# Kernel optimization log

Measured on AMD Instinct MI355X. Metric: run time of the kernel, lower is better.

## Reference

```python
import jax, jax.numpy as jnp
import numpy as np

N_NODES = 50000
N_EDGES = 1600000
IN_F = 512
OUT_F = 256


def setup_inputs() -> dict:
    key = jax.random.key(0)
    k1, k2, k3, k4, k5 = jax.random.split(key, 5)
    features = jax.random.normal(k1, (N_NODES, IN_F), dtype=jnp.float32)
    # xavier_uniform init for weight [in_features, out_features]
    limit = np.sqrt(6.0 / (IN_F + OUT_F)).astype(np.float32)
    weight = jax.random.uniform(k2, (IN_F, OUT_F), dtype=jnp.float32,
                                minval=-limit, maxval=limit)
    # COO sparse adjacency (normalized edge weights in [0,1))
    edge_vals = jax.random.uniform(k3, (N_EDGES,), dtype=jnp.float32)
    edge_rows = jax.random.randint(k4, (N_EDGES,), 0, N_NODES, dtype=jnp.int32)
    edge_cols = jax.random.randint(k5, (N_EDGES,), 0, N_NODES, dtype=jnp.int32)
    return {"features": features, "weight": weight, "edge_vals": edge_vals,
            "edge_rows": edge_rows, "edge_cols": edge_cols}


def reference(features, weight, edge_vals, edge_rows, edge_cols):
    # dropout p=0.0 / eval mode -> identity
    support = features @ weight                      # [N, out_f] dense GEMM
    # torch.spmm(adj, support): out[r] += val * support[c] for each edge (r, c)
    gathered = support[edge_cols] * edge_vals[:, None]   # [E, out_f]
    output = jax.ops.segment_sum(gathered, edge_rows, num_segments=N_NODES)
    return jax.nn.relu(output)
```

## Files before the change

kernel.cpp:

```cpp
#include <hip/hip_runtime.h>

#define N_NODES 50000
#define N_EDGES 1600000
#define IN_F    512
#define OUT_F   256

#define BROWS   128
#define NBINS   ((N_NODES + BROWS - 1) / BROWS)
#define BATCH   4096
#define NBATCHES ((N_EDGES + BATCH - 1) / BATCH)
#define EPT     (BATCH / 256)

typedef __attribute__((ext_vector_type(8))) short bf16x8;
typedef __attribute__((ext_vector_type(4))) float f32x4;
typedef unsigned long long ull;

__device__ __forceinline__ short bf16rne(float f) {
    unsigned u = __builtin_bit_cast(unsigned, f);
    u += 0x7fffu + ((u >> 16) & 1u);
    return (short)(u >> 16);
}

__device__ __forceinline__ float b2f(unsigned short h) {
    unsigned u = (unsigned)h << 16;
    return __builtin_bit_cast(float, u);
}

__global__ __launch_bounds__(256) void wt_kernel(const float* __restrict__ W,
                                                 short* __restrict__ Wt) {
    int idx = blockIdx.x * 256 + threadIdx.x;
    if (idx < IN_F * OUT_F) {
        int n = idx >> 9;
        int k = idx & 511;
        Wt[idx] = bf16rne(W[(size_t)k * OUT_F + n]);
    }
}

#define ASTRIDE 40
#define BSTRIDE 40

__global__ __launch_bounds__(512) void gemm_mfma_kernel(const float* __restrict__ A,
                                                        const short* __restrict__ Wt,
                                                        unsigned short* __restrict__ Cb) {
    __shared__ short As[128 * ASTRIDE];
    __shared__ short Bs[256 * BSTRIDE];

    const int tid  = threadIdx.x;
    const int wave = tid >> 6;
    const int lane = tid & 63;
    const int m0   = blockIdx.x * 128;
    const int wrow = (wave >> 2) * 64;
    const int wcol = (wave & 3) * 64;

    const int quad = lane >> 4;
    const int l16  = lane & 15;

    const int ar = tid >> 2;
    const int aq = tid & 3;

    const int bn = tid >> 1;
    const int bh = tid & 1;

    f32x4 zero4 = {0.f, 0.f, 0.f, 0.f};
    f32x4 acc[4][4];
#pragma unroll
    for (int i = 0; i < 4; ++i)
#pragma unroll
        for (int j = 0; j < 4; ++j) acc[i][j] = zero4;

    for (int k0 = 0; k0 < IN_F; k0 += 32) {
        {
            const int gm = m0 + ar;
            float4 v0 = make_float4(0.f, 0.f, 0.f, 0.f);
            float4 v1 = v0;
            if (gm < N_NODES) {
                const float* p = A + (size_t)gm * IN_F + k0 + aq * 8;
                v0 = *(const float4*)p;
                v1 = *(const float4*)(p + 4);
            }
            bf16x8 b;
            b[0] = bf16rne(v0.x); b[1] = bf16rne(v0.y);
            b[2] = bf16rne(v0.z); b[3] = bf16rne(v0.w);
            b[4] = bf16rne(v1.x); b[5] = bf16rne(v1.y);
            b[6] = bf16rne(v1.z); b[7] = bf16rne(v1.w);
            *(bf16x8*)&As[ar * ASTRIDE + aq * 8] = b;
        }
        {
            const short* src = Wt + (size_t)bn * IN_F + k0 + bh * 16;
            bf16x8 w0 = *(const bf16x8*)(src + 0);
            bf16x8 w1 = *(const bf16x8*)(src + 8);
            short* dst = &Bs[bn * BSTRIDE + bh * 16];
            *(bf16x8*)(dst + 0) = w0;
            *(bf16x8*)(dst + 8) = w1;
        }
        __syncthreads();

        bf16x8 af[4], bf[4];
#pragma unroll
        for (int mt = 0; mt < 4; ++mt)
            af[mt] = *(const bf16x8*)&As[(wrow + mt * 16 + l16) * ASTRIDE + quad * 8];
#pragma unroll
        for (int nt = 0; nt < 4; ++nt)
            bf[nt] = *(const bf16x8*)&Bs[(wcol + nt * 16 + l16) * BSTRIDE + quad * 8];

#pragma unroll
        for (int mt = 0; mt < 4; ++mt)
#pragma unroll
            for (int nt = 0; nt < 4; ++nt)
                acc[mt][nt] = __builtin_amdgcn_mfma_f32_16x16x32_bf16(
                    af[mt], bf[nt], acc[mt][nt], 0, 0, 0);
        __syncthreads();
    }

#pragma unroll
    for (int mt = 0; mt < 4; ++mt) {
        const int rbase = m0 + wrow + mt * 16 + quad * 4;
#pragma unroll
        for (int i = 0; i < 4; ++i) {
            const int row = rbase + i;
            if (row < N_NODES) {
#pragma unroll
                for (int nt = 0; nt < 4; ++nt)
                    Cb[(size_t)row * OUT_F + wcol + nt * 16 + l16] =
                        (unsigned short)bf16rne(acc[mt][nt][i]);
            }
        }
    }
}

__global__ __launch_bounds__(256) void quant_kernel(const ushort4* __restrict__ sup16,
                                                    unsigned int* __restrict__ sup8,
                                                    float* __restrict__ scales) {
    const int tid  = threadIdx.x;
    const int row  = blockIdx.x * 4 + (tid >> 6);
    const int lane = tid & 63;
    if (row >= N_NODES) return;

    const ushort4 v = sup16[(size_t)row * 64 + lane];
    const float a0 = b2f(v.x), a1 = b2f(v.y), a2 = b2f(v.z), a3 = b2f(v.w);
    float m = fmaxf(fmaxf(fabsf(a0), fabsf(a1)), fmaxf(fabsf(a2), fabsf(a3)));
#pragma unroll
    for (int off = 32; off >= 1; off >>= 1)
        m = fmaxf(m, __shfl_xor(m, off, 64));

    const float inv = (m > 0.f) ? 127.f / m : 0.f;
    const int q0 = (int)rintf(a0 * inv) + 128;
    const int q1 = (int)rintf(a1 * inv) + 128;
    const int q2 = (int)rintf(a2 * inv) + 128;
    const int q3 = (int)rintf(a3 * inv) + 128;
    sup8[(size_t)row * 64 + lane] =
        (unsigned)q0 | ((unsigned)q1 << 8) | ((unsigned)q2 << 16) | ((unsigned)q3 << 24);
    if (lane == 0) scales[row] = m * (1.f / 127.f);
}

__global__ __launch_bounds__(256) void zero_bins_kernel(int* __restrict__ binCounts,
                                                        int* __restrict__ relCur) {
    int i = blockIdx.x * 256 + threadIdx.x;
    if (i < NBINS) { binCounts[i] = 0; relCur[i] = 0; }
}

__global__ __launch_bounds__(256) void histA_kernel(const int* __restrict__ rows,
                                                    int* __restrict__ binCounts) {
    __shared__ int lh[NBINS];
    const int tid = threadIdx.x;
    for (int i = tid; i < NBINS; i += 256) lh[i] = 0;
    __syncthreads();
    for (int i = blockIdx.x * 256 + tid; i < N_EDGES; i += gridDim.x * 256)
        atomicAdd(&lh[rows[i] >> 7], 1);
    __syncthreads();
    for (int i = tid; i < NBINS; i += 256)
        if (lh[i]) atomicAdd(&binCounts[i], lh[i]);
}

__global__ __launch_bounds__(256) void fillA_kernel(const int* __restrict__ rows,
                                                    const int* __restrict__ cols,
                                                    const float* __restrict__ vals,
                                                    const int* __restrict__ binCounts,
                                                    int* __restrict__ relCur,
                                                    int* __restrict__ binStart,
                                                    int2* __restrict__ binned) {
    __shared__ int lhist[NBINS];
    __shared__ int lexcl[NBINS];
    __shared__ int gbase[NBINS];
    __shared__ ull stmp2[256];
    __shared__ int2 lstage[BATCH];
    __shared__ unsigned short sbucket[BATCH];

    const int tid   = threadIdx.x;
    const int start = blockIdx.x * BATCH;
    const int count = min(BATCH, N_EDGES - start);

    for (int i = tid; i < NBINS; i += 256) lhist[i] = 0;
    __syncthreads();

    int myrow[EPT], myrank[EPT];
#pragma unroll
    for (int j = 0; j < EPT; ++j) {
        const int s = j * 256 + tid;
        if (s < count) {
            const int r = rows[start + s];
            myrow[j]  = r;
            myrank[j] = atomicAdd(&lhist[r >> 7], 1);
        }
    }
    __syncthreads();

    {
        const int i0 = 2 * tid, i1 = 2 * tid + 1;
        const int h0 = (i0 < NBINS) ? lhist[i0] : 0;
        const int h1 = (i1 < NBINS) ? lhist[i1] : 0;
        const int c0 = (i0 < NBINS) ? binCounts[i0] : 0;
        const int c1 = (i1 < NBINS) ? binCounts[i1] : 0;
        const ull pair = ((ull)(unsigned)(c0 + c1) << 32) | (unsigned)(h0 + h1);
        stmp2[tid] = pair;
        for (int off = 1; off < 256; off <<= 1) {
            __syncthreads();
            ull t = (tid >= off) ? stmp2[tid - off] : 0ull;
            __syncthreads();
            stmp2[tid] += t;
        }
        __syncthreads();
        const ull pex  = stmp2[tid] - pair;
        const int lex0 = (int)(pex & 0xffffffffull);
        const int bst0 = (int)(pex >> 32);
        if (i0 < NBINS) {
            lexcl[i0] = lex0;
            gbase[i0] = bst0 + (h0 ? atomicAdd(&relCur[i0], h0) : 0);
            if (blockIdx.x == 0) binStart[i0] = bst0;
        }
        if (i1 < NBINS) {
            lexcl[i1] = lex0 + h0;
            gbase[i1] = (bst0 + c0) + (h1 ? atomicAdd(&relCur[i1], h1) : 0);
            if (blockIdx.x == 0) binStart[i1] = bst0 + c0;
        }
    }
    __syncthreads();

#pragma unroll
    for (int j = 0; j < EPT; ++j) {
        const int s = j * 256 + tid;
        if (s < count) {
            const int r   = myrow[j];
            const int b   = r >> 7;
            const int pos = lexcl[b] + myrank[j];
            lstage[pos]  = make_int2(((r & 127) << 16) | cols[start + s],
                                     __float_as_int(vals[start + s]));
            sbucket[pos] = (unsigned short)b;
        }
    }
    __syncthreads();

#pragma unroll
    for (int j = 0; j < EPT; ++j) {
        const int s = j * 256 + tid;
        if (s < count) {
            const int b = sbucket[s];
            binned[gbase[b] + (s - lexcl[b])] = lstage[s];
        }
    }
}

__global__ __launch_bounds__(512) void sortB_kernel(const int2* __restrict__ binned,
                                                    const int* __restrict__ binStart,
                                                    const int* __restrict__ binCounts,
                                                    int* __restrict__ excl,
                                                    unsigned int* __restrict__ ecv) {
    __shared__ int lhist[BROWS];
    __shared__ int lcur[BROWS];

    const int tid  = threadIdx.x;
    const int b    = blockIdx.x;
    const int base = binStart[b];
    const int cnt  = binCounts[b];

    if (tid < BROWS) lhist[tid] = 0;
    __syncthreads();

    for (int i = tid; i < cnt; i += 512)
        atomicAdd(&lhist[binned[base + i].x >> 16], 1);
    __syncthreads();

    if (tid < BROWS) lcur[tid] = lhist[tid];
    for (int off = 1; off < BROWS; off <<= 1) {
        __syncthreads();
        int t = (tid >= off && tid < BROWS) ? lcur[tid - off] : 0;
        __syncthreads();
        if (tid < BROWS) lcur[tid] += t;
    }
    __syncthreads();
    if (tid < BROWS) {
        const int pexcl = lcur[tid] - lhist[tid];
        const int row   = b * BROWS + tid;
        lcur[tid] = pexcl;
        if (row < N_NODES) excl[row] = base + pexcl;
    }
    __syncthreads();

    for (int i = tid; i < cnt; i += 512) {
        const int2 e  = binned[base + i];
        const int rl  = e.x >> 16;
        const int col = e.x & 0xFFFF;
        const int rank = atomicAdd(&lcur[rl], 1);
        ecv[base + rank] = ((unsigned int)col << 16) |
                           (unsigned short)bf16rne(__int_as_float(e.y));
    }
}

__global__ __launch_bounds__(256) void gather_kernel(const unsigned int* __restrict__ support,
                                                     const float* __restrict__ scales,
                                                     const int* __restrict__ excl,
                                                     const unsigned int* __restrict__ ecv,
                                                     float4* __restrict__ out) {
    const int tid  = threadIdx.x;
    const int row  = blockIdx.x * 4 + (tid >> 6);
    const int lane = tid & 63;
    if (row >= N_NODES) return;

    const int start = excl[row];
    const int end   = (row + 1 < N_NODES) ? excl[row + 1] : N_EDGES;

    float4 acc = make_float4(0.f, 0.f, 0.f, 0.f);
    float csum = 0.f;
    int e = start;
    const int end4 = start + ((end - start) & ~3);
    for (; e < end4; e += 4) {
        const unsigned int p0 = ecv[e];
        const unsigned int p1 = ecv[e + 1];
        const unsigned int p2 = ecv[e + 2];
        const unsigned int p3 = ecv[e + 3];
        const int c0 = p0 >> 16, c1 = p1 >> 16, c2 = p2 >> 16, c3 = p3 >> 16;
        const unsigned int u0 = support[(size_t)c0 * 64 + lane];
        const unsigned int u1 = support[(size_t)c1 * 64 + lane];
        const unsigned int u2 = support[(size_t)c2 * 64 + lane];
        const unsigned int u3 = support[(size_t)c3 * 64 + lane];
        const float v0 = b2f((unsigned short)(p0 & 0xFFFF)) * scales[c0];
        const float v1 = b2f((unsigned short)(p1 & 0xFFFF)) * scales[c1];
        const float v2 = b2f((unsigned short)(p2 & 0xFFFF)) * scales[c2];
        const float v3 = b2f((unsigned short)(p3 & 0xFFFF)) * scales[c3];
        csum += v0 + v1 + v2 + v3;
        acc.x += v0 * (float)(u0 & 0xff)         + v1 * (float)(u1 & 0xff)
               + v2 * (float)(u2 & 0xff)         + v3 * (float)(u3 & 0xff);
        acc.y += v0 * (float)((u0 >> 8) & 0xff)  + v1 * (float)((u1 >> 8) & 0xff)
               + v2 * (float)((u2 >> 8) & 0xff)  + v3 * (float)((u3 >> 8) & 0xff);
        acc.z += v0 * (float)((u0 >> 16) & 0xff) + v1 * (float)((u1 >> 16) & 0xff)
               + v2 * (float)((u2 >> 16) & 0xff) + v3 * (float)((u3 >> 16) & 0xff);
        acc.w += v0 * (float)(u0 >> 24)          + v1 * (float)(u1 >> 24)
               + v2 * (float)(u2 >> 24)          + v3 * (float)(u3 >> 24);
    }
    for (; e < end; ++e) {
        const unsigned int p0 = ecv[e];
        const int c0 = p0 >> 16;
        const unsigned int u0 = support[(size_t)c0 * 64 + lane];
        const float v0 = b2f((unsigned short)(p0 & 0xFFFF)) * scales[c0];
        csum += v0;
        acc.x += v0 * (float)(u0 & 0xff);
        acc.y += v0 * (float)((u0 >> 8) & 0xff);
        acc.z += v0 * (float)((u0 >> 16) & 0xff);
        acc.w += v0 * (float)(u0 >> 24);
    }

    const float bias = 128.f * csum;
    acc.x = fmaxf(acc.x - bias, 0.f);
    acc.y = fmaxf(acc.y - bias, 0.f);
    acc.z = fmaxf(acc.z - bias, 0.f);
    acc.w = fmaxf(acc.w - bias, 0.f);
    out[(size_t)row * 64 + lane] = acc;
}

extern "C" void kernel_launch(void* const* d_in, const int* in_sizes, int n_in,
                              void* d_out, int out_size, void* d_ws, size_t ws_size,
                              hipStream_t stream) {
    const float* features  = (const float*)d_in[0];
    const float* weight    = (const float*)d_in[1];
    const float* edge_vals = (const float*)d_in[2];
    const int*   edge_rows = (const int*)d_in[3];
    const int*   edge_cols = (const int*)d_in[4];
    float* out = (float*)d_out;

    unsigned short* support_bf = (unsigned short*)d_ws;
    int2*  binned    = (int2*)(support_bf + (size_t)N_NODES * OUT_F);
    unsigned int* ecv = (unsigned int*)(binned + N_EDGES);
    int*   excl      = (int*)(ecv + N_EDGES);
    int*   binCounts = excl + N_NODES;
    int*   binStart  = binCounts + 512;
    int*   relCur    = binStart + 512;
    float* scales    = (float*)(relCur + 512);
    short* Wt        = (short*)(scales + N_NODES);
    unsigned int* support_i8 = (unsigned int*)binned;

    wt_kernel<<<(IN_F * OUT_F + 255) / 256, 256, 0, stream>>>(weight, Wt);

    gemm_mfma_kernel<<<(N_NODES + 127) / 128, 512, 0, stream>>>(features, Wt, support_bf);

    zero_bins_kernel<<<2, 256, 0, stream>>>(binCounts, relCur);
    histA_kernel<<<256, 256, 0, stream>>>(edge_rows, binCounts);
    fillA_kernel<<<NBATCHES, 256, 0, stream>>>(edge_rows, edge_cols, edge_vals,
                                               binCounts, relCur, binStart, binned);
    sortB_kernel<<<NBINS, 512, 0, stream>>>(binned, binStart, binCounts, excl, ecv);

    quant_kernel<<<(N_NODES + 3) / 4, 256, 0, stream>>>(
        (const ushort4*)support_bf, support_i8, scales);

    gather_kernel<<<(N_NODES + 3) / 4, 256, 0, stream>>>(
        support_i8, scales, excl, ecv, (float4*)out);
}
```

Baseline: 327.8 us.

## Fuse int8 row quantization into GEMM epilogue and fold scales into edge values

The GEMM epilogue now computes per-row absmax through a shuffle and shared-memory reduction and writes int8 support plus per-row scales directly, removing the separate bf16 support write and the quant kernel pass. The sort kernel premultiplies each edge value by its column's scale, so the gather no longer loads scales per edge. The trade-offs are a slightly heavier GEMM epilogue with an extra block barrier, byte-wide scattered stores, and an extra rounding step because the scaled value is stored in bf16.

```diff
diff --git a/kernel.cpp b/kernel.cpp
--- a/kernel.cpp
+++ b/kernel.cpp
@@ -41,9 +41,11 @@
 
 __global__ __launch_bounds__(512) void gemm_mfma_kernel(const float* __restrict__ A,
                                                         const short* __restrict__ Wt,
-                                                        unsigned short* __restrict__ Cb) {
+                                                        unsigned char* __restrict__ Cb8,
+                                                        float* __restrict__ scales) {
     __shared__ short As[128 * ASTRIDE];
     __shared__ short Bs[256 * BSTRIDE];
+    __shared__ float redmax[128][5];
 
     const int tid  = threadIdx.x;
     const int wave = tid >> 6;
@@ -112,45 +114,54 @@
         __syncthreads();
     }
 
+    float pm[4][4];
+#pragma unroll
+    for (int mt = 0; mt < 4; ++mt)
+#pragma unroll
+        for (int i = 0; i < 4; ++i) {
+            float m = fabsf(acc[mt][0][i]);
+            m = fmaxf(m, fabsf(acc[mt][1][i]));
+            m = fmaxf(m, fabsf(acc[mt][2][i]));
+            m = fmaxf(m, fabsf(acc[mt][3][i]));
+            pm[mt][i] = m;
+        }
+#pragma unroll
+    for (int off = 1; off < 16; off <<= 1)
+#pragma unroll
+        for (int mt = 0; mt < 4; ++mt)
+#pragma unroll
+            for (int i = 0; i < 4; ++i)
+                pm[mt][i] = fmaxf(pm[mt][i], __shfl_xor(pm[mt][i], off, 64));
+
+    if (l16 == 0) {
+#pragma unroll
+        for (int mt = 0; mt < 4; ++mt)
+#pragma unroll
+            for (int i = 0; i < 4; ++i)
+                redmax[wrow + mt * 16 + quad * 4 + i][wave & 3] = pm[mt][i];
+    }
+    __syncthreads();
+
 #pragma unroll
     for (int mt = 0; mt < 4; ++mt) {
-        const int rbase = m0 + wrow + mt * 16 + quad * 4;
 #pragma unroll
         for (int i = 0; i < 4; ++i) {
-            const int row = rbase + i;
+            const int rl  = wrow + mt * 16 + quad * 4 + i;
+            const int row = m0 + rl;
             if (row < N_NODES) {
-#pragma unroll
-                for (int nt = 0; nt < 4; ++nt)
-                    Cb[(size_t)row * OUT_F + wcol + nt * 16 + l16] =
-                        (unsigned short)bf16rne(acc[mt][nt][i]);
+                const float m = fmaxf(fmaxf(redmax[rl][0], redmax[rl][1]),
+                                      fmaxf(redmax[rl][2], redmax[rl][3]));
+                const float inv = (m > 0.f) ? 127.f / m : 0.f;
+#pragma unroll
+                for (int nt = 0; nt < 4; ++nt) {
+                    const int q = (int)rintf(acc[mt][nt][i] * inv) + 128;
+                    Cb8[(size_t)row * OUT_F + wcol + nt * 16 + l16] = (unsigned char)q;
+                }
+                if ((wave & 3) == 0 && l16 == 0)
+                    scales[row] = m * (1.f / 127.f);
             }
         }
     }
-}
-
-__global__ __launch_bounds__(256) void quant_kernel(const ushort4* __restrict__ sup16,
-                                                    unsigned int* __restrict__ sup8,
-                                                    float* __restrict__ scales) {
-    const int tid  = threadIdx.x;
-    const int row  = blockIdx.x * 4 + (tid >> 6);
-    const int lane = tid & 63;
-    if (row >= N_NODES) return;
-
-    const ushort4 v = sup16[(size_t)row * 64 + lane];
-    const float a0 = b2f(v.x), a1 = b2f(v.y), a2 = b2f(v.z), a3 = b2f(v.w);
-    float m = fmaxf(fmaxf(fabsf(a0), fabsf(a1)), fmaxf(fabsf(a2), fabsf(a3)));
-#pragma unroll
-    for (int off = 32; off >= 1; off >>= 1)
-        m = fmaxf(m, __shfl_xor(m, off, 64));
-
-    const float inv = (m > 0.f) ? 127.f / m : 0.f;
-    const int q0 = (int)rintf(a0 * inv) + 128;
-    const int q1 = (int)rintf(a1 * inv) + 128;
-    const int q2 = (int)rintf(a2 * inv) + 128;
-    const int q3 = (int)rintf(a3 * inv) + 128;
-    sup8[(size_t)row * 64 + lane] =
-        (unsigned)q0 | ((unsigned)q1 << 8) | ((unsigned)q2 << 16) | ((unsigned)q3 << 24);
-    if (lane == 0) scales[row] = m * (1.f / 127.f);
 }
 
 __global__ __launch_bounds__(256) void zero_bins_kernel(int* __restrict__ binCounts,
@@ -263,6 +274,7 @@
 __global__ __launch_bounds__(512) void sortB_kernel(const int2* __restrict__ binned,
                                                     const int* __restrict__ binStart,
                                                     const int* __restrict__ binCounts,
+                                                    const float* __restrict__ scales,
                                                     int* __restrict__ excl,
                                                     unsigned int* __restrict__ ecv) {
     __shared__ int lhist[BROWS];
@@ -301,13 +313,13 @@
         const int rl  = e.x >> 16;
         const int col = e.x & 0xFFFF;
         const int rank = atomicAdd(&lcur[rl], 1);
+        const float vs = __int_as_float(e.y) * scales[col];
         ecv[base + rank] = ((unsigned int)col << 16) |
-                           (unsigned short)bf16rne(__int_as_float(e.y));
+                           (unsigned short)bf16rne(vs);
     }
 }
 
 __global__ __launch_bounds__(256) void gather_kernel(const unsigned int* __restrict__ support,
-                                                     const float* __restrict__ scales,
                                                      const int* __restrict__ excl,
                                                      const unsigned int* __restrict__ ecv,
                                                      float4* __restrict__ out) {
@@ -328,15 +340,14 @@
         const unsigned int p1 = ecv[e + 1];
         const unsigned int p2 = ecv[e + 2];
         const unsigned int p3 = ecv[e + 3];
-        const int c0 = p0 >> 16, c1 = p1 >> 16, c2 = p2 >> 16, c3 = p3 >> 16;
-        const unsigned int u0 = support[(size_t)c0 * 64 + lane];
-        const unsigned int u1 = support[(size_t)c1 * 64 + lane];
-        const unsigned int u2 = support[(size_t)c2 * 64 + lane];
-        const unsigned int u3 = support[(size_t)c3 * 64 + lane];
-        const float v0 = b2f((unsigned short)(p0 & 0xFFFF)) * scales[c0];
-        const float v1 = b2f((unsigned short)(p1 & 0xFFFF)) * scales[c1];
-        const float v2 = b2f((unsigned short)(p2 & 0xFFFF)) * scales[c2];
-        const float v3 = b2f((unsigned short)(p3 & 0xFFFF)) * scales[c3];
+        const unsigned int u0 = support[(size_t)(p0 >> 16) * 64 + lane];
+        const unsigned int u1 = support[(size_t)(p1 >> 16) * 64 + lane];
+        const unsigned int u2 = support[(size_t)(p2 >> 16) * 64 + lane];
+        const unsigned int u3 = support[(size_t)(p3 >> 16) * 64 + lane];
+        const float v0 = b2f((unsigned short)(p0 & 0xFFFF));
+        const float v1 = b2f((unsigned short)(p1 & 0xFFFF));
+        const float v2 = b2f((unsigned short)(p2 & 0xFFFF));
+        const float v3 = b2f((unsigned short)(p3 & 0xFFFF));
         csum += v0 + v1 + v2 + v3;
         acc.x += v0 * (float)(u0 & 0xff)         + v1 * (float)(u1 & 0xff)
                + v2 * (float)(u2 & 0xff)         + v3 * (float)(u3 & 0xff);
@@ -349,9 +360,8 @@
     }
     for (; e < end; ++e) {
         const unsigned int p0 = ecv[e];
-        const int c0 = p0 >> 16;
-        const unsigned int u0 = support[(size_t)c0 * 64 + lane];
-        const float v0 = b2f((unsigned short)(p0 & 0xFFFF)) * scales[c0];
+        const unsigned int u0 = support[(size_t)(p0 >> 16) * 64 + lane];
+        const float v0 = b2f((unsigned short)(p0 & 0xFFFF));
         csum += v0;
         acc.x += v0 * (float)(u0 & 0xff);
         acc.y += v0 * (float)((u0 >> 8) & 0xff);
@@ -377,8 +387,8 @@
     const int*   edge_cols = (const int*)d_in[4];
     float* out = (float*)d_out;
 
-    unsigned short* support_bf = (unsigned short*)d_ws;
-    int2*  binned    = (int2*)(support_bf + (size_t)N_NODES * OUT_F);
+    unsigned int* support_i8 = (unsigned int*)d_ws;
+    int2*  binned    = (int2*)(support_i8 + (size_t)N_NODES * 64);
     unsigned int* ecv = (unsigned int*)(binned + N_EDGES);
     int*   excl      = (int*)(ecv + N_EDGES);
     int*   binCounts = excl + N_NODES;
@@ -386,21 +396,19 @@
     int*   relCur    = binStart + 512;
     float* scales    = (float*)(relCur + 512);
     short* Wt        = (short*)(scales + N_NODES);
-    unsigned int* support_i8 = (unsigned int*)binned;
 
     wt_kernel<<<(IN_F * OUT_F + 255) / 256, 256, 0, stream>>>(weight, Wt);
 
-    gemm_mfma_kernel<<<(N_NODES + 127) / 128, 512, 0, stream>>>(features, Wt, support_bf);
+    gemm_mfma_kernel<<<(N_NODES + 127) / 128, 512, 0, stream>>>(
+        features, Wt, (unsigned char*)support_i8, scales);
 
     zero_bins_kernel<<<2, 256, 0, stream>>>(binCounts, relCur);
     histA_kernel<<<256, 256, 0, stream>>>(edge_rows, binCounts);
     fillA_kernel<<<NBATCHES, 256, 0, stream>>>(edge_rows, edge_cols, edge_vals,
                                                binCounts, relCur, binStart, binned);
-    sortB_kernel<<<NBINS, 512, 0, stream>>>(binned, binStart, binCounts, excl, ecv);
-
-    quant_kernel<<<(N_NODES + 3) / 4, 256, 0, stream>>>(
-        (const ushort4*)support_bf, support_i8, scales);
+    sortB_kernel<<<NBINS, 512, 0, stream>>>(binned, binStart, binCounts, scales,
+                                            excl, ecv);
 
     gather_kernel<<<(N_NODES + 3) / 4, 256, 0, stream>>>(
-        support_i8, scales, excl, ecv, (float4*)out);
-}
+        support_i8, excl, ecv, (float4*)out);
+}
```

New measurement: 322.8 us. About the same (-1.5%).
